# Kernel tuning notes

Hardware: AMD Instinct MI355X
Metric: run time of the kernel (lower is better)

Reference implementation:

```python
import jax, jax.numpy as jnp
import numpy as np

V, H, L, T = 32000, 1024, 256, 4096


def setup_inputs() -> dict:
    key = jax.random.key(0)
    ks = jax.random.split(key, 16)
    s_h = 1.0 / np.sqrt(H)
    return {
        "tokens": jax.random.randint(ks[0], (T,), 0, V, dtype=jnp.int64),
        "h0": jnp.zeros((1, 1, H), jnp.float32),
        "c0": jnp.zeros((1, 1, H), jnp.float32),
        "embedding": jax.random.normal(ks[1], (V, H), jnp.float32),
        "w_ih": jax.random.uniform(ks[2], (4 * H, H), jnp.float32, -s_h, s_h),
        "w_hh": jax.random.uniform(ks[3], (4 * H, H), jnp.float32, -s_h, s_h),
        "b_ih": jax.random.uniform(ks[4], (4 * H,), jnp.float32, -s_h, s_h),
        "b_hh": jax.random.uniform(ks[5], (4 * H,), jnp.float32, -s_h, s_h),
        "W_hm": jax.random.uniform(ks[6], (L, H), jnp.float32, -s_h, s_h),
        "b_hm": jax.random.uniform(ks[7], (L,), jnp.float32, -s_h, s_h),
        "W_hv": jax.random.uniform(ks[8], (L, H), jnp.float32, -s_h, s_h),
        "b_hv": jax.random.uniform(ks[9], (L,), jnp.float32, -s_h, s_h),
        "W_cm": jax.random.uniform(ks[10], (L, H), jnp.float32, -s_h, s_h),
        "b_cm": jax.random.uniform(ks[11], (L,), jnp.float32, -s_h, s_h),
        "W_cv": jax.random.uniform(ks[12], (L, H), jnp.float32, -s_h, s_h),
        "b_cv": jax.random.uniform(ks[13], (L,), jnp.float32, -s_h, s_h),
    }


def reference(tokens, h0, c0, embedding, w_ih, w_hh, b_ih, b_hh,
              W_hm, b_hm, W_hv, b_hv, W_cm, b_cm, W_cv, b_cv):
    # embedding lookup: (T, H)
    emb = embedding[tokens]
    # precompute input-side gate projections for all timesteps (one GEMM)
    x_gates = emb @ w_ih.T + (b_ih + b_hh)  # (T, 4H)

    def step(carry, xg):
        h, c = carry  # each (H,)
        gates = xg + h @ w_hh.T  # (4H,)
        i, f, g, o = jnp.split(gates, 4)
        i = jax.nn.sigmoid(i)
        f = jax.nn.sigmoid(f)
        g = jnp.tanh(g)
        o = jax.nn.sigmoid(o)
        c = f * c + i * g
        h = o * jnp.tanh(c)
        return (h, c), None

    (h, c), _ = jax.lax.scan(step, (h0.reshape(-1), c0.reshape(-1)), x_gates)
    finalHidden = h.reshape(1, 1, -1)
    finalCell = c.reshape(1, 1, -1)
    hidden_mean = finalHidden @ W_hm.T + b_hm
    hidden_logVar = finalHidden @ W_hv.T + b_hv
    cell_mean = finalCell @ W_cm.T + b_cm
    cell_logVar = finalCell @ W_cv.T + b_cv
    return (hidden_mean, hidden_logVar, cell_mean, cell_logVar)
```

## Files before the change

### kernel.cpp

```cpp
#include <hip/hip_runtime.h>
#include <math.h>

#define T_SEQ 4096
#define H_DIM 1024
#define G4    4096
#define NBLK  64
#define NTHR  512
#define SCAN_LDS_BYTES (131072 + 2048 + 4096)

typedef __fp16 half2_t __attribute__((ext_vector_type(2)));
union U32H2 { unsigned u; half2_t h; };
__device__ __forceinline__ half2_t as_h2(unsigned u) { U32H2 c; c.u = u; return c.h; }
__device__ __forceinline__ unsigned pkh2(float a, float b) {
    U32H2 c; c.h = __builtin_amdgcn_cvt_pkrtz(a, b); return c.u;
}

__global__ __launch_bounds__(256) void xg_gemm(
    const int* __restrict__ tokens, const float* __restrict__ emb,
    const float* __restrict__ w_ih, const float* __restrict__ b_ih,
    const float* __restrict__ b_hh, float* __restrict__ xg)
{
    __shared__ float As[16][128];
    __shared__ float Bs[16][128];
    __shared__ int   tk[128];

    const int tid  = threadIdx.x;
    const int row0 = blockIdx.y * 128;
    const int col0 = blockIdx.x * 128;

    if (tid < 128) tk[tid] = tokens[row0 + tid];
    __syncthreads();

    const int r    = tid >> 1;
    const int half = tid & 1;
    const int tx   = tid & 15;
    const int ty   = tid >> 4;

    const float* ap_base = emb + (size_t)tk[r] * 1024 + half * 8;
    const float* bp_base = w_ih + (size_t)(col0 + r) * 1024 + half * 8;

    float acc[8][8] = {};

    for (int kc = 0; kc < 1024; kc += 16) {
        const float4 a0 = ((const float4*)(ap_base + kc))[0];
        const float4 a1 = ((const float4*)(ap_base + kc))[1];
        const float4 b0 = ((const float4*)(bp_base + kc))[0];
        const float4 b1 = ((const float4*)(bp_base + kc))[1];
        __syncthreads();
        const int kb = half * 8;
        As[kb+0][r] = a0.x; As[kb+1][r] = a0.y; As[kb+2][r] = a0.z; As[kb+3][r] = a0.w;
        As[kb+4][r] = a1.x; As[kb+5][r] = a1.y; As[kb+6][r] = a1.z; As[kb+7][r] = a1.w;
        Bs[kb+0][r] = b0.x; Bs[kb+1][r] = b0.y; Bs[kb+2][r] = b0.z; Bs[kb+3][r] = b0.w;
        Bs[kb+4][r] = b1.x; Bs[kb+5][r] = b1.y; Bs[kb+6][r] = b1.z; Bs[kb+7][r] = b1.w;
        __syncthreads();
        #pragma unroll
        for (int k = 0; k < 16; ++k) {
            const float4 a0v = *(const float4*)&As[k][ty*8];
            const float4 a1v = *(const float4*)&As[k][ty*8+4];
            const float4 b0v = *(const float4*)&Bs[k][tx*8];
            const float4 b1v = *(const float4*)&Bs[k][tx*8+4];
            const float aa[8] = {a0v.x,a0v.y,a0v.z,a0v.w,a1v.x,a1v.y,a1v.z,a1v.w};
            const float bb[8] = {b0v.x,b0v.y,b0v.z,b0v.w,b1v.x,b1v.y,b1v.z,b1v.w};
            #pragma unroll
            for (int ii = 0; ii < 8; ++ii)
                #pragma unroll
                for (int jj = 0; jj < 8; ++jj)
                    acc[ii][jj] = fmaf(aa[ii], bb[jj], acc[ii][jj]);
        }
    }

    const int ccol = col0 + tx * 8;
    float bs[8];
    #pragma unroll
    for (int jj = 0; jj < 8; ++jj) bs[jj] = b_ih[ccol + jj] + b_hh[ccol + jj];
    #pragma unroll
    for (int ii = 0; ii < 8; ++ii) {
        float* orow = xg + (size_t)(row0 + ty*8 + ii) * G4 + ccol;
        float4 o0, o1;
        o0.x = acc[ii][0] + bs[0]; o0.y = acc[ii][1] + bs[1];
        o0.z = acc[ii][2] + bs[2]; o0.w = acc[ii][3] + bs[3];
        o1.x = acc[ii][4] + bs[4]; o1.y = acc[ii][5] + bs[5];
        o1.z = acc[ii][6] + bs[6]; o1.w = acc[ii][7] + bs[7];
        ((float4*)orow)[0] = o0;
        ((float4*)orow)[1] = o1;
    }
}

__device__ __forceinline__ float fsigmoid_(float x) {
    return 1.0f / (1.0f + __expf(-x));
}
__device__ __forceinline__ float ftanh_(float x) {
    x = fminf(fmaxf(x, -10.0f), 10.0f);
    const float e = __expf(2.0f * x);
    return (e - 1.0f) / (e + 1.0f);
}

__global__ __launch_bounds__(NTHR, 1) void lstm_scan(
    const float* __restrict__ xg, const float* __restrict__ w_hh,
    const float* __restrict__ h0, const float* __restrict__ c0,
    unsigned long long* h_msg,
    float* __restrict__ h_fin, float* __restrict__ c_fin)
{
    extern __shared__ char smem[];
    unsigned* w_lds = (unsigned*)smem;
    unsigned* hbuf  = (unsigned*)(smem + 131072);
    float*    dpart = (float*)(smem + 131072 + 2048);

    const int tid  = threadIdx.x;
    const int b    = blockIdx.x;
    const int wv   = tid >> 6;
    const int lane = tid & 63;

    {
        const int grow = (lane >> 4) * 1024 + 16 * b + (lane & 15);
        const float* wsrc = w_hh + (size_t)grow * 1024 + wv * 128;
        uint4* wdst = (uint4*)w_lds + wv * 1024 + lane;
        #pragma unroll
        for (int i = 0; i < 16; ++i) {
            const float4 a = ((const float4*)wsrc)[2 * i];
            const float4 d = ((const float4*)wsrc)[2 * i + 1];
            uint4 u;
            u.x = pkh2(a.x, a.y); u.y = pkh2(a.z, a.w);
            u.z = pkh2(d.x, d.y); u.w = pkh2(d.z, d.w);
            wdst[i * 64] = u;
        }
    }

    float c_reg = 0.0f;
    if (tid < 16) c_reg = c0[16 * b + tid];
    float xc = 0.0f;
    if (tid < 64) xc = xg[(size_t)(tid >> 4) * 1024 + 16 * b + (tid & 15)];

    {
        const float2 hh = ((const float2*)h0)[wv * 64 + lane];
        hbuf[wv * 64 + lane] = pkh2(hh.x, hh.y);
    }
    __syncthreads();

    const uint4* wrd = (const uint4*)w_lds + wv * 1024 + lane;
    const uint4* h4  = (const uint4*)hbuf + wv * 16;

    uint4 wreg[16];
    #pragma unroll
    for (int i = 0; i < 16; ++i) wreg[i] = wrd[i * 64];

    for (int t = 0; t < T_SEQ; ++t) {
        if (t > 0) {
            const unsigned ver = (unsigned)t;
            const unsigned long long* base = h_msg + (size_t)(t & 1) * H_DIM;

            {
                const unsigned long long* s = base + 128 * wv + 16 * lane;
                for (;;) {
                    unsigned tg = ver;
                    if (lane < 8)
                        tg = (unsigned)(__hip_atomic_load(s, __ATOMIC_RELAXED,
                                                          __HIP_MEMORY_SCOPE_AGENT) >> 32);
                    if (__all(tg == ver)) break;
                    __builtin_amdgcn_s_sleep(1);
                }
            }
            const unsigned long long* src = base + 128 * wv + 2 * lane;
            unsigned long long v0, v1;
            for (;;) {
                v0 = __hip_atomic_load(src + 0, __ATOMIC_RELAXED, __HIP_MEMORY_SCOPE_AGENT);
                v1 = __hip_atomic_load(src + 1, __ATOMIC_RELAXED, __HIP_MEMORY_SCOPE_AGENT);
                if (((unsigned)(v0 >> 32) == ver) & ((unsigned)(v1 >> 32) == ver))
                    break;
            }
            hbuf[wv * 64 + lane] = pkh2(__uint_as_float((unsigned)v0),
                                        __uint_as_float((unsigned)v1));
        }
        asm volatile("s_waitcnt lgkmcnt(0)" ::: "memory");
        __builtin_amdgcn_wave_barrier();
        __builtin_amdgcn_sched_barrier(0);

        float acc = 0.0f;
        #pragma unroll
        for (int i = 0; i < 16; ++i) {
            const uint4 uw = wreg[i];
            const uint4 uh = h4[i];
            acc = __builtin_amdgcn_fdot2(as_h2(uw.x), as_h2(uh.x), acc, false);
            acc = __builtin_amdgcn_fdot2(as_h2(uw.y), as_h2(uh.y), acc, false);
            acc = __builtin_amdgcn_fdot2(as_h2(uw.z), as_h2(uh.z), acc, false);
            acc = __builtin_amdgcn_fdot2(as_h2(uw.w), as_h2(uh.w), acc, false);
        }
        dpart[(t & 1) * 512 + wv * 64 + lane] = acc;

        #pragma unroll
        for (int i = 0; i < 16; ++i) wreg[i] = wrd[i * 64];

        float xn = 0.0f;
        if ((tid < 64) & (t < T_SEQ - 1))
            xn = xg[(size_t)(t + 1) * G4 + (tid >> 4) * 1024 + 16 * b + (tid & 15)];

        __syncthreads();

        if (tid < 64) {
            const float* dp = dpart + (t & 1) * 512;
            float x = xc;
            #pragma unroll
            for (int w8 = 0; w8 < 8; ++w8) x += dp[w8 * 64 + tid];
            const float act = ((tid >> 4) == 2) ? ftanh_(x) : fsigmoid_(x);
            const int m = tid & 15;
            const float a_i = __shfl(act, m, 64);
            const float a_f = __shfl(act, m + 16, 64);
            const float a_g = __shfl(act, m + 32, 64);
            const float a_o = __shfl(act, m + 48, 64);
            if (tid < 16) {
                c_reg = a_f * c_reg + a_i * a_g;
                const float hn = a_o * ftanh_(c_reg);
                if (t < T_SEQ - 1) {
                    const unsigned long long msg =
                        ((unsigned long long)(unsigned)(t + 1) << 32) | __float_as_uint(hn);
                    __hip_atomic_store(&h_msg[(size_t)((t + 1) & 1) * H_DIM + 16 * b + tid],
                                       msg, __ATOMIC_RELAXED, __HIP_MEMORY_SCOPE_AGENT);
                } else {
                    h_fin[16 * b + tid] = hn;
                    c_fin[16 * b + tid] = c_reg;
                }
            }
        }
        xc = xn;
    }
}

__global__ __launch_bounds__(256) void proj_kernel(
    const float* __restrict__ h_fin, const float* __restrict__ c_fin,
    const float* __restrict__ W_hm, const float* __restrict__ b_hm,
    const float* __restrict__ W_hv, const float* __restrict__ b_hv,
    const float* __restrict__ W_cm, const float* __restrict__ b_cm,
    const float* __restrict__ W_cv, const float* __restrict__ b_cv,
    float* __restrict__ out)
{
    const int tid = threadIdx.x;
    const int g32 = tid >> 5;
    const int j   = tid & 31;
    const int o   = blockIdx.x * 8 + g32;
    const int mat = o >> 8;
    const int l   = o & 255;

    const float* W;  const float* bias;  const float* vec;
    if      (mat == 0) { W = W_hm; bias = b_hm; vec = h_fin; }
    else if (mat == 1) { W = W_hv; bias = b_hv; vec = h_fin; }
    else if (mat == 2) { W = W_cm; bias = b_cm; vec = c_fin; }
    else               { W = W_cv; bias = b_cv; vec = c_fin; }

    const float* wrow = W + (size_t)l * 1024;
    float acc = 0.0f;
    #pragma unroll
    for (int i = 0; i < 8; ++i) {
        const float4 wv = *(const float4*)(wrow + i * 128 + j * 4);
        const float4 xv = *(const float4*)(vec  + i * 128 + j * 4);
        acc += wv.x * xv.x + wv.y * xv.y + wv.z * xv.z + wv.w * xv.w;
    }
    acc += __shfl_xor(acc, 1);
    acc += __shfl_xor(acc, 2);
    acc += __shfl_xor(acc, 4);
    acc += __shfl_xor(acc, 8);
    acc += __shfl_xor(acc, 16);
    if (j == 0) out[o] = acc + bias[l];
}

extern "C" void kernel_launch(void* const* d_in, const int* in_sizes, int n_in,
                              void* d_out, int out_size, void* d_ws, size_t ws_size,
                              hipStream_t stream)
{
    const int*   tokens = (const int*)  d_in[0];
    const float* h0     = (const float*)d_in[1];
    const float* c0     = (const float*)d_in[2];
    const float* emb    = (const float*)d_in[3];
    const float* w_ih   = (const float*)d_in[4];
    const float* w_hh   = (const float*)d_in[5];
    const float* b_ih   = (const float*)d_in[6];
    const float* b_hh   = (const float*)d_in[7];
    const float* W_hm   = (const float*)d_in[8];
    const float* b_hm   = (const float*)d_in[9];
    const float* W_hv   = (const float*)d_in[10];
    const float* b_hv   = (const float*)d_in[11];
    const float* W_cm   = (const float*)d_in[12];
    const float* b_cm   = (const float*)d_in[13];
    const float* W_cv   = (const float*)d_in[14];
    const float* b_cv   = (const float*)d_in[15];
    float* out = (float*)d_out;

    char* ws = (char*)d_ws;
    float*              xg    = (float*)ws;
    size_t              off   = (size_t)T_SEQ * G4 * sizeof(float);
    unsigned long long* h_msg = (unsigned long long*)(ws + off);
    off += 2 * H_DIM * sizeof(unsigned long long);
    float* h_fin = (float*)(ws + off); off += H_DIM * sizeof(float);
    float* c_fin = (float*)(ws + off); off += H_DIM * sizeof(float);

    (void)hipFuncSetAttribute((const void*)lstm_scan,
                              hipFuncAttributeMaxDynamicSharedMemorySize,
                              SCAN_LDS_BYTES);

    hipMemsetAsync(h_msg, 0xFF, 2 * H_DIM * sizeof(unsigned long long), stream);

    xg_gemm<<<dim3(32, 32), 256, 0, stream>>>(tokens, emb, w_ih, b_ih, b_hh, xg);
    lstm_scan<<<NBLK, NTHR, SCAN_LDS_BYTES, stream>>>(xg, w_hh, h0, c0, h_msg,
                                                      h_fin, c_fin);
    proj_kernel<<<128, 256, 0, stream>>>(h_fin, c_fin, W_hm, b_hm, W_hv, b_hv,
                                         W_cm, b_cm, W_cv, b_cv, out);
}
```

Measured before the change: 8.026 ms.

## Use fp16 dot2 in input GEMM and drop sentinel pre-poll in scan

Result: faster. 7.242 ms (-9.8%).

```diff
diff --git a/kernel.cpp b/kernel.cpp
--- a/kernel.cpp
+++ b/kernel.cpp
@@ -20,9 +20,9 @@
     const float* __restrict__ w_ih, const float* __restrict__ b_ih,
     const float* __restrict__ b_hh, float* __restrict__ xg)
 {
-    __shared__ float As[16][128];
-    __shared__ float Bs[16][128];
-    __shared__ int   tk[128];
+    __shared__ unsigned As2[8][128];
+    __shared__ unsigned Bs2[8][128];
+    __shared__ int      tk[128];
 
     const int tid  = threadIdx.x;
     const int row0 = blockIdx.y * 128;
@@ -47,25 +47,29 @@
         const float4 b0 = ((const float4*)(bp_base + kc))[0];
         const float4 b1 = ((const float4*)(bp_base + kc))[1];
         __syncthreads();
-        const int kb = half * 8;
-        As[kb+0][r] = a0.x; As[kb+1][r] = a0.y; As[kb+2][r] = a0.z; As[kb+3][r] = a0.w;
-        As[kb+4][r] = a1.x; As[kb+5][r] = a1.y; As[kb+6][r] = a1.z; As[kb+7][r] = a1.w;
-        Bs[kb+0][r] = b0.x; Bs[kb+1][r] = b0.y; Bs[kb+2][r] = b0.z; Bs[kb+3][r] = b0.w;
-        Bs[kb+4][r] = b1.x; Bs[kb+5][r] = b1.y; Bs[kb+6][r] = b1.z; Bs[kb+7][r] = b1.w;
+        const int kb = half * 4;
+        As2[kb+0][r] = pkh2(a0.x, a0.y);
+        As2[kb+1][r] = pkh2(a0.z, a0.w);
+        As2[kb+2][r] = pkh2(a1.x, a1.y);
+        As2[kb+3][r] = pkh2(a1.z, a1.w);
+        Bs2[kb+0][r] = pkh2(b0.x, b0.y);
+        Bs2[kb+1][r] = pkh2(b0.z, b0.w);
+        Bs2[kb+2][r] = pkh2(b1.x, b1.y);
+        Bs2[kb+3][r] = pkh2(b1.z, b1.w);
         __syncthreads();
         #pragma unroll
-        for (int k = 0; k < 16; ++k) {
-            const float4 a0v = *(const float4*)&As[k][ty*8];
-            const float4 a1v = *(const float4*)&As[k][ty*8+4];
-            const float4 b0v = *(const float4*)&Bs[k][tx*8];
-            const float4 b1v = *(const float4*)&Bs[k][tx*8+4];
-            const float aa[8] = {a0v.x,a0v.y,a0v.z,a0v.w,a1v.x,a1v.y,a1v.z,a1v.w};
-            const float bb[8] = {b0v.x,b0v.y,b0v.z,b0v.w,b1v.x,b1v.y,b1v.z,b1v.w};
+        for (int kk = 0; kk < 8; ++kk) {
+            unsigned aa[8], bb[8];
+            #pragma unroll
+            for (int ii = 0; ii < 8; ++ii) aa[ii] = As2[kk][ty*8 + ii];
+            #pragma unroll
+            for (int jj = 0; jj < 8; ++jj) bb[jj] = Bs2[kk][tx*8 + jj];
             #pragma unroll
             for (int ii = 0; ii < 8; ++ii)
                 #pragma unroll
                 for (int jj = 0; jj < 8; ++jj)
-                    acc[ii][jj] = fmaf(aa[ii], bb[jj], acc[ii][jj]);
+                    acc[ii][jj] = __builtin_amdgcn_fdot2(
+                        as_h2(aa[ii]), as_h2(bb[jj]), acc[ii][jj], false);
         }
     }
 
@@ -147,20 +151,8 @@
     for (int t = 0; t < T_SEQ; ++t) {
         if (t > 0) {
             const unsigned ver = (unsigned)t;
-            const unsigned long long* base = h_msg + (size_t)(t & 1) * H_DIM;
-
-            {
-                const unsigned long long* s = base + 128 * wv + 16 * lane;
-                for (;;) {
-                    unsigned tg = ver;
-                    if (lane < 8)
-                        tg = (unsigned)(__hip_atomic_load(s, __ATOMIC_RELAXED,
-                                                          __HIP_MEMORY_SCOPE_AGENT) >> 32);
-                    if (__all(tg == ver)) break;
-                    __builtin_amdgcn_s_sleep(1);
-                }
-            }
-            const unsigned long long* src = base + 128 * wv + 2 * lane;
+            const unsigned long long* src =
+                h_msg + (size_t)(t & 1) * H_DIM + 128 * wv + 2 * lane;
             unsigned long long v0, v1;
             for (;;) {
                 v0 = __hip_atomic_load(src + 0, __ATOMIC_RELAXED, __HIP_MEMORY_SCOPE_AGENT);
```
